# Performance work log

Hardware: AMD Instinct MI355X
Metric: run time of the kernel (lower is better)

The kernel has to match this reference:

```python
import jax, jax.numpy as jnp
import numpy as np

FACTOR = 5  # ProbAttention factor


def setup_inputs() -> dict:
    key = jax.random.key(0)
    kq, kk, kv = jax.random.split(key, 3)
    B, H, D, L = 4, 8, 64, 4096
    return {
        "queries": jax.random.normal(kq, (B, H, D, L), jnp.float32),
        "keys": jax.random.normal(kk, (B, H, D, L), jnp.float32),
        "values": jax.random.normal(kv, (B, H, D, L), jnp.float32),
        "attn_mask": jnp.zeros((1,), jnp.bool_),  # unused when mask_flag=True (recomputed internally)
    }


def reference(queries, keys, values, attn_mask):
    B, H, D, L_Q = queries.shape  # input layout [B, H, D, L]
    q = jnp.transpose(queries, (0, 1, 3, 2))  # [B,H,L,D]
    k = jnp.transpose(keys, (0, 1, 3, 2))
    v = jnp.transpose(values, (0, 1, 3, 2))
    L_K = k.shape[2]  # true key length (used inside _prob_QK)
    # --- faithful bug from original: L_K/L_V read from queries' LAST dim (=D) ---
    L_K_bug = D
    L_V_bug = D
    U_part = FACTOR * int(np.ceil(np.log(L_K_bug)))
    U_part = U_part if U_part < L_K_bug else L_K_bug  # sample_k
    u = FACTOR * int(np.ceil(np.log(L_Q)))
    u = u if u < L_Q else L_Q  # n_top
    # scaling (bugged denominators for k, v)
    q = q / (np.sqrt(D) * np.sqrt(L_Q))
    k = k / (np.sqrt(D) * np.sqrt(L_K_bug))
    v = v / (np.sqrt(D) * np.sqrt(L_V_bug))

    # ---- _prob_QK: sampled QK, top-u query selection ----
    skey = jax.random.key(42)  # fixed key: deterministic stand-in for torch.randint
    index_sample = jax.random.randint(skey, (L_Q, U_part), 0, L_K)  # [L_Q, U_part]
    K_sample = k[:, :, index_sample, :]  # [B,H,L_Q,U_part,D]
    Q_K_sample = jnp.einsum('bhld,bhlsd->bhls', q, K_sample)  # [B,H,L_Q,U_part]
    M = Q_K_sample.max(-1) - Q_K_sample.sum(-1) / L_K  # sparsity measure, real L_K here
    _, M_top = jax.lax.top_k(M, u)  # [B,H,u] (order irrelevant: distinct scatter targets)
    Q_reduce = jnp.take_along_axis(q, M_top[..., None], axis=2)  # [B,H,u,D]
    scores = jnp.einsum('bhud,bhkd->bhuk', Q_reduce, k)  # [B,H,u,L_K]

    scale = 1.0 / (np.sqrt(D) * np.sqrt(L_Q))  # self.scale is None
    scores = scores * scale

    # ---- initial context (mask_flag=True -> causal cumsum) ----
    context = jnp.cumsum(v, axis=2)  # [B,H,L_Q,D]

    # ---- ProbMask + update ----
    causal = jnp.triu(jnp.ones((L_Q, L_K), jnp.bool_), 1)  # [L_Q, L_K]
    indicator = causal[M_top]  # [B,H,u,L_K]
    scores = jnp.where(indicator, -jnp.inf, scores)
    attn = jax.nn.softmax(scores, axis=-1)
    upd = jnp.einsum('bhuk,bhkd->bhud', attn, v)  # [B,H,u,D]
    bi = jnp.arange(B)[:, None, None]
    hi = jnp.arange(H)[None, :, None]
    context = context.at[bi, hi, M_top].set(upd)

    out = jnp.transpose(context, (0, 1, 3, 2)).reshape(queries.shape)
    return out
```

## Files before the change

### kernel.cpp

```cpp
#include <hip/hip_runtime.h>
#include <cstdint>

constexpr int B_ = 4, H_ = 8, D_ = 64, L_ = 4096;
constexpr int BH = B_ * H_;
constexpr int U_PART = 25;
constexpr int TOPU = 45;
constexpr int CHUNK = 128;
constexpr int NCH = L_ / CHUNK;
constexpr int PSTRIDE = 68;

#define JAX_THREEFRY_PARTITIONABLE 1

__host__ __device__ inline void tf2x32(uint32_t k0, uint32_t k1,
                                       uint32_t x0, uint32_t x1,
                                       uint32_t& y0, uint32_t& y1) {
  const uint32_t ks2 = k0 ^ k1 ^ 0x1BD11BDAu;
  uint32_t v0 = x0 + k0, v1 = x1 + k1;
#define RND(r) { v0 += v1; v1 = (v1 << (r)) | (v1 >> (32 - (r))); v1 ^= v0; }
  RND(13) RND(15) RND(26) RND(6)
  v0 += k1; v1 += ks2 + 1u;
  RND(17) RND(29) RND(16) RND(24)
  v0 += ks2; v1 += k0 + 2u;
  RND(13) RND(15) RND(26) RND(6)
  v0 += k0; v1 += k1 + 3u;
  RND(17) RND(29) RND(16) RND(24)
  v0 += k1; v1 += ks2 + 4u;
  RND(13) RND(15) RND(26) RND(6)
  v0 += ks2; v1 += k0 + 5u;
#undef RND
  y0 = v0; y1 = v1;
}

__global__ __launch_bounds__(256) void sample_idx_kernel(int* __restrict__ idx,
                                                         uint32_t k2a, uint32_t k2b) {
#if JAX_THREEFRY_PARTITIONABLE
  int i = blockIdx.x * 256 + threadIdx.x;
  if (i >= L_ * U_PART) return;
  uint32_t y0, y1;
  tf2x32(k2a, k2b, 0u, (uint32_t)i, y0, y1);
  idx[i] = (int)((y0 ^ y1) & 4095u);
#else
  int j = blockIdx.x * 256 + threadIdx.x;
  const int half = (L_ * U_PART) / 2;
  if (j >= half) return;
  uint32_t y0, y1;
  tf2x32(k2a, k2b, (uint32_t)j, (uint32_t)(j + half), y0, y1);
  idx[j] = (int)(y0 & 4095u);
  idx[j + half] = (int)(y1 & 4095u);
#endif
}

__global__ __launch_bounds__(256) void transpose_cumsum(
    const float* __restrict__ q, const float* __restrict__ k, const float* __restrict__ v,
    float* __restrict__ qt, float* __restrict__ kt, float* __restrict__ out) {
  const int bh = blockIdx.y;
  const int t = threadIdx.x;
  if (blockIdx.z == 2) {
    const int row = bh * D_ + blockIdx.x;
    const float* src = v + (size_t)row * L_;
    float* dst = out + (size_t)row * L_;
    float vals[16];
    const float4* s4 = (const float4*)(src + t * 16);
#pragma unroll
    for (int i = 0; i < 4; i++) {
      float4 x = s4[i];
      vals[4 * i + 0] = x.x; vals[4 * i + 1] = x.y;
      vals[4 * i + 2] = x.z; vals[4 * i + 3] = x.w;
    }
    float run = 0.0f;
#pragma unroll
    for (int i = 0; i < 16; i++) { run += vals[i] * (1.0f / 64.0f); vals[i] = run; }
    float x = run;
#pragma unroll
    for (int off = 1; off < 64; off <<= 1) {
      float y = __shfl_up(x, off, 64);
      if ((t & 63) >= off) x += y;
    }
    __shared__ float wtot[4];
    if ((t & 63) == 63) wtot[t >> 6] = x;
    __syncthreads();
    float woff = 0.0f;
    for (int w = 0; w < (t >> 6); w++) woff += wtot[w];
    const float excl = x - run + woff;
#pragma unroll
    for (int i = 0; i < 16; i++) vals[i] += excl;
    float4* d4 = (float4*)(dst + t * 16);
#pragma unroll
    for (int i = 0; i < 4; i++)
      d4[i] = make_float4(vals[4 * i], vals[4 * i + 1], vals[4 * i + 2], vals[4 * i + 3]);
    return;
  }
  const float* src; float* dst; float scale;
  if (blockIdx.z == 0) { src = q; dst = qt; scale = 1.0f / 512.0f; }
  else                 { src = k; dst = kt; scale = 1.0f / 64.0f; }
  const int l0 = blockIdx.x * 64;
  __shared__ float tile[64][65];
  const float* s = src + (size_t)bh * D_ * L_ + l0;
  float* d = dst + (size_t)bh * L_ * D_;
  const int rhi = t >> 4, rlo = t & 15;
#pragma unroll
  for (int i = 0; i < 4; i++) {
    const int dd = i * 16 + rhi;
    float4 x = *(const float4*)&s[(size_t)dd * L_ + 4 * rlo];
    tile[dd][4 * rlo + 0] = x.x * scale;
    tile[dd][4 * rlo + 1] = x.y * scale;
    tile[dd][4 * rlo + 2] = x.z * scale;
    tile[dd][4 * rlo + 3] = x.w * scale;
  }
  __syncthreads();
#pragma unroll
  for (int i = 0; i < 4; i++) {
    const int ll = i * 16 + rhi;
    float4 o;
    o.x = tile[4 * rlo + 0][ll];
    o.y = tile[4 * rlo + 1][ll];
    o.z = tile[4 * rlo + 2][ll];
    o.w = tile[4 * rlo + 3][ll];
    *(float4*)&d[(size_t)(l0 + ll) * D_ + 4 * rlo] = o;
  }
}

__device__ __forceinline__ float dpp_bcast_add16(float x) {
  int xi;
  xi = __builtin_amdgcn_mov_dpp(__float_as_int(x), 0x140, 0xF, 0xF, true);
  x += __int_as_float(xi);
  xi = __builtin_amdgcn_mov_dpp(__float_as_int(x), 0x141, 0xF, 0xF, true);
  x += __int_as_float(xi);
  xi = __builtin_amdgcn_mov_dpp(__float_as_int(x), 0x4E, 0xF, 0xF, true);
  x += __int_as_float(xi);
  xi = __builtin_amdgcn_mov_dpp(__float_as_int(x), 0xB1, 0xF, 0xF, true);
  x += __int_as_float(xi);
  return x;
}

__global__ __launch_bounds__(256) void m_kernel(const float* __restrict__ qt,
                                                const float* __restrict__ kt,
                                                const int* __restrict__ idx,
                                                float* __restrict__ M) {
  const int t = threadIdx.x;
  const int w = t >> 6, lane = t & 63;
  const int g = lane >> 4, gl = lane & 15;
  const int xcd = blockIdx.x & 7;
  const int slot = blockIdx.x >> 3;
  const int bh = xcd * 4 + (slot >> 8);
  const int lg = slot & 255;
  const int l = lg * 16 + w * 4 + g;
  const int gidx = bh * L_ + l;
  const float* qtb = qt + (size_t)bh * L_ * D_;
  const float* ktb = kt + (size_t)bh * L_ * D_;
  const float4 ql = *(const float4*)(qtb + (size_t)l * D_ + gl * 4);
  const int* ip = idx + l * U_PART;
  float mx = -INFINITY, sm = 0.0f;
#pragma unroll 5
  for (int s = 0; s < U_PART; s++) {
    int ki = ip[s];
    float4 kk = *(const float4*)(ktb + (size_t)ki * D_ + gl * 4);
    float p = ql.x * kk.x + ql.y * kk.y + ql.z * kk.z + ql.w * kk.w;
    p = dpp_bcast_add16(p);
    mx = fmaxf(mx, p);
    sm += p;
  }
  if (gl == 0) M[gidx] = mx - sm * (1.0f / 4096.0f);
}

__global__ __launch_bounds__(256) void topk_kernel(const float* __restrict__ M,
                                                   int* __restrict__ ssel_g) {
  const int bh = blockIdx.x, t = threadIdx.x;
  const int w = t >> 6, lane = t & 63;
  const float* Mb = M + (size_t)bh * L_;
  const int base = w * 1024 + lane;
  uint32_t v[16];
#pragma unroll
  for (int j = 0; j < 16; j++) {
    uint32_t b = __float_as_uint(Mb[base + j * 64]);
    v[j] = b ^ ((b & 0x80000000u) ? 0xFFFFFFFFu : 0x80000000u);
  }
  __shared__ unsigned long long red[4];
  __shared__ int picks[TOPU];
  for (int it = 0; it < TOPU; it++) {
    unsigned long long best = 0ull;
#pragma unroll
    for (int j = 0; j < 16; j++) {
      unsigned long long key = ((unsigned long long)v[j] << 32)
                             | (uint32_t)(L_ - 1 - (base + j * 64));
      best = (key > best) ? key : best;
    }
#pragma unroll
    for (int off = 32; off; off >>= 1) {
      unsigned long long o = __shfl_xor(best, off, 64);
      best = (o > best) ? o : best;
    }
    if (lane == 0) red[w] = best;
    __syncthreads();
    unsigned long long g = red[0];
    if (red[1] > g) g = red[1];
    if (red[2] > g) g = red[2];
    if (red[3] > g) g = red[3];
    const int bi = L_ - 1 - (int)(g & 0xFFFFFFFFu);
    if (t == 0) picks[it] = bi;
    if ((bi >> 10) == w && (bi & 63) == lane) {
      const int slot = (bi >> 6) & 15;
#pragma unroll
      for (int j = 0; j < 16; j++) if (slot == j) v[j] = 0u;
    }
    __syncthreads();
  }
  if (t < TOPU) {
    int my = picks[t];
    int rank = 0;
    for (int j = 0; j < TOPU; j++) rank += (picks[j] > my);
    ssel_g[bh * TOPU + rank] = my;
  }
}

__global__ __launch_bounds__(256) void update_partial(const float* __restrict__ qt,
                                                      const float* __restrict__ kraw,
                                                      const float* __restrict__ vraw,
                                                      const int* __restrict__ ssel_g,
                                                      float* __restrict__ part) {
  const int xcd = blockIdx.x & 7;
  const int slot = blockIdx.x >> 3;
  const int bh = xcd * 4 + (slot >> 4);
  const int ch0 = slot & 15;
  const int t = threadIdx.x;
  const int w = t >> 6, lane = t & 63;
  const int kl = lane & 15, rg = lane >> 4;

  __shared__ float kv[CHUNK * 64];
  __shared__ float qs[48 * 68];
  __shared__ float eS[48 * 132];
  __shared__ int ssel[48];

  if (t < 48) ssel[t] = (t < TOPU) ? ssel_g[bh * TOPU + t] : -1;
  __syncthreads();

#pragma unroll
  for (int j = 0; j < 3; j++) {
    int it = t + 256 * j;
    int rr = it >> 4, dc = it & 15;
    int sel = ssel[rr];
    float4 qv = make_float4(0.f, 0.f, 0.f, 0.f);
    if (sel >= 0) qv = *(const float4*)&qt[((size_t)bh * L_ + sel) * D_ + 4 * dc];
    *(float4*)&qs[rr * 68 + 4 * dc] = qv;
  }

  for (int pass = 0; pass < 2; pass++) {
    const int ch = pass ? (31 - ch0) : ch0;
    const int k0 = ch * CHUNK;
    int lo = 0, hi = TOPU;
    while (lo < hi) { int mid = (lo + hi) >> 1; if (ssel[mid] >= k0) lo = mid + 1; else hi = mid; }
    const int nact = lo;
    if (nact == 0) continue;

    __syncthreads();
    const float* kb = kraw + (size_t)bh * D_ * L_ + k0;
#pragma unroll
    for (int j = 0; j < 8; j++) {
      int e4 = 4 * (t + 256 * j);
      int d = e4 >> 7, key = e4 & 127;
      *(float4*)&kv[e4] = *(const float4*)&kb[(size_t)d * L_ + key];
    }
    __syncthreads();

    const int wr0 = 12 * w;
    if (wr0 < nact) {
      float s[3][8];
#pragma unroll
      for (int j = 0; j < 3; j++)
#pragma unroll
        for (int x = 0; x < 8; x++) s[j][x] = 0.f;
#pragma unroll 8
      for (int d = 0; d < 64; d++) {
        float4 ka = *(const float4*)&kv[d * 128 + 4 * kl];
        float4 kb2 = *(const float4*)&kv[d * 128 + 64 + 4 * kl];
#pragma unroll
        for (int j = 0; j < 3; j++) {
          float qd = qs[(wr0 + 3 * rg + j) * 68 + d];
          s[j][0] += qd * ka.x;  s[j][1] += qd * ka.y;
          s[j][2] += qd * ka.z;  s[j][3] += qd * ka.w;
          s[j][4] += qd * kb2.x; s[j][5] += qd * kb2.y;
          s[j][6] += qd * kb2.z; s[j][7] += qd * kb2.w;
        }
      }
#pragma unroll
      for (int j = 0; j < 3; j++) {
        const int R = wr0 + 3 * rg + j;
        const int sel = ssel[R];
        float mx = -INFINITY;
#pragma unroll
        for (int x = 0; x < 8; x++) {
          int kg = k0 + 4 * kl + (x < 4 ? x : 60 + x);
          s[j][x] *= (1.0f / 32768.0f);
          if (kg > sel) s[j][x] = -INFINITY;
          mx = fmaxf(mx, s[j][x]);
        }
        mx = fmaxf(mx, __shfl_xor(mx, 1, 64));
        mx = fmaxf(mx, __shfl_xor(mx, 2, 64));
        mx = fmaxf(mx, __shfl_xor(mx, 4, 64));
        mx = fmaxf(mx, __shfl_xor(mx, 8, 64));
        float e[8], sm = 0.f;
#pragma unroll
        for (int x = 0; x < 8; x++) { e[x] = expf(s[j][x] - mx); sm += e[x]; }
        sm += __shfl_xor(sm, 1, 64);
        sm += __shfl_xor(sm, 2, 64);
        sm += __shfl_xor(sm, 4, 64);
        sm += __shfl_xor(sm, 8, 64);
        *(float4*)&eS[R * 132 + 4 * kl] = make_float4(e[0], e[1], e[2], e[3]);
        *(float4*)&eS[R * 132 + 64 + 4 * kl] = make_float4(e[4], e[5], e[6], e[7]);
        if (kl == 0 && R < nact) {
          float* p = part + ((size_t)(bh * TOPU + R) * NCH + ch) * PSTRIDE;
          p[64] = mx; p[65] = sm;
        }
      }
    }
    __syncthreads();
    const float* vb = vraw + (size_t)bh * D_ * L_ + k0;
#pragma unroll
    for (int j = 0; j < 8; j++) {
      int e4 = 4 * (t + 256 * j);
      int d = e4 >> 7, kq = (e4 & 127) >> 2;
      float4 vv = *(const float4*)&vb[(size_t)d * L_ + 4 * kq];
      *(float4*)&kv[d * 128 + ((kq ^ (d & 31)) << 2)] = vv;
    }
    __syncthreads();
    if (wr0 < nact) {
      float acc[3][4];
#pragma unroll
      for (int j = 0; j < 3; j++)
#pragma unroll
        for (int x = 0; x < 4; x++) acc[j][x] = 0.f;
      const int dbase = 4 * kl;
#pragma unroll 4
      for (int kb = 0; kb < 32; kb++) {
        float4 ev[3];
#pragma unroll
        for (int j = 0; j < 3; j++)
          ev[j] = *(const float4*)&eS[(wr0 + 3 * rg + j) * 132 + 4 * kb];
#pragma unroll
        for (int x = 0; x < 4; x++) {
          const int dx = dbase + x;
          float4 vv = *(const float4*)&kv[dx * 128 + ((kb ^ (dx & 31)) << 2)];
#pragma unroll
          for (int j = 0; j < 3; j++) {
            acc[j][x] += ev[j].x * vv.x + ev[j].y * vv.y
                       + ev[j].z * vv.z + ev[j].w * vv.w;
          }
        }
      }
#pragma unroll
      for (int j = 0; j < 3; j++) {
        const int R = wr0 + 3 * rg + j;
        if (R < nact) {
          float* p = part + ((size_t)(bh * TOPU + R) * NCH + ch) * PSTRIDE;
          float4 o = make_float4(acc[j][0] * (1.0f / 64.0f), acc[j][1] * (1.0f / 64.0f),
                                 acc[j][2] * (1.0f / 64.0f), acc[j][3] * (1.0f / 64.0f));
          *(float4*)&p[4 * kl] = o;
        }
      }
    }
  }
}

__global__ __launch_bounds__(256) void update_combine(const float* __restrict__ part,
                                                      const int* __restrict__ ssel_g,
                                                      float* __restrict__ out) {
  const int row = blockIdx.x * 4 + (threadIdx.x >> 6);
  if (row >= BH * TOPU) return;
  const int bh = row / TOPU;
  const int sel = ssel_g[row];
  const int d = threadIdx.x & 63;
  const int nv = sel / CHUNK + 1;
  const float* p = part + (size_t)row * NCH * PSTRIDE;

  float m = -INFINITY;
  for (int c = 0; c < nv; c++) m = fmaxf(m, p[c * PSTRIDE + 64]);

  float num = 0.0f, den = 0.0f;
  for (int c = 0; c < nv; c++) {
    float mc = p[c * PSTRIDE + 64];
    float wgt = expf(mc - m);
    num += wgt * p[c * PSTRIDE + d];
    den += wgt * p[c * PSTRIDE + 65];
  }
  out[((size_t)bh * D_ + d) * L_ + sel] = num / den;
}

extern "C" void kernel_launch(void* const* d_in, const int* in_sizes, int n_in,
                              void* d_out, int out_size, void* d_ws, size_t ws_size,
                              hipStream_t stream) {
  const float* q = (const float*)d_in[0];
  const float* k = (const float*)d_in[1];
  const float* v = (const float*)d_in[2];
  float* out = (float*)d_out;

  const size_t NT = (size_t)BH * L_ * D_;
  float* qt = (float*)d_ws;
  float* kt = qt + NT;
  float* M  = kt + NT;
  int* idx  = (int*)(M + (size_t)BH * L_);
  int* ssel = idx + L_ * U_PART;
  float* part = (float*)(ssel + BH * TOPU);

  uint32_t k2a, k2b;
#if JAX_THREEFRY_PARTITIONABLE
  tf2x32(0u, 42u, 0u, 1u, k2a, k2b);
#else
  uint32_t a0, a1, b0, b1;
  tf2x32(0u, 42u, 0u, 2u, a0, a1);
  tf2x32(0u, 42u, 1u, 3u, b0, b1);
  k2a = a1; k2b = b1;
#endif

#if JAX_THREEFRY_PARTITIONABLE
  sample_idx_kernel<<<(L_ * U_PART + 255) / 256, 256, 0, stream>>>(idx, k2a, k2b);
#else
  sample_idx_kernel<<<(L_ * U_PART / 2 + 255) / 256, 256, 0, stream>>>(idx, k2a, k2b);
#endif
  transpose_cumsum<<<dim3(L_ / 64, BH, 3), 256, 0, stream>>>(q, k, v, qt, kt, out);
  m_kernel<<<BH * L_ / 16, 256, 0, stream>>>(qt, kt, idx, M);
  topk_kernel<<<BH, 256, 0, stream>>>(M, ssel);
  update_partial<<<BH * 16, 256, 0, stream>>>(qt, k, v, ssel, part);
  update_combine<<<(BH * TOPU + 3) / 4, 256, 0, stream>>>(part, ssel, out);
}
```

Before: 171.1 us.

## Fuse Q transpose into M kernel and fold index sampling into cumsum blocks

Removes the global transposed copy of Q. The M kernel now transposes and scales its own 64-row Q tile in shared memory and processes four query rows per group. The top-k kernel gathers and scales the selected query rows into a small buffer for the update stage. The random sample-index generation moves into the cumsum blocks of the transpose kernel, which drops one kernel launch and a full write and read of Q. The cost is more work per block in the M kernel, and the top-k gather does strided reads from raw Q.

```diff
diff --git a/kernel.cpp b/kernel.cpp
--- a/kernel.cpp
+++ b/kernel.cpp
@@ -31,31 +31,32 @@
   y0 = v0; y1 = v1;
 }
 
-__global__ __launch_bounds__(256) void sample_idx_kernel(int* __restrict__ idx,
-                                                         uint32_t k2a, uint32_t k2b) {
-#if JAX_THREEFRY_PARTITIONABLE
-  int i = blockIdx.x * 256 + threadIdx.x;
-  if (i >= L_ * U_PART) return;
-  uint32_t y0, y1;
-  tf2x32(k2a, k2b, 0u, (uint32_t)i, y0, y1);
-  idx[i] = (int)((y0 ^ y1) & 4095u);
-#else
-  int j = blockIdx.x * 256 + threadIdx.x;
-  const int half = (L_ * U_PART) / 2;
-  if (j >= half) return;
-  uint32_t y0, y1;
-  tf2x32(k2a, k2b, (uint32_t)j, (uint32_t)(j + half), y0, y1);
-  idx[j] = (int)(y0 & 4095u);
-  idx[j + half] = (int)(y1 & 4095u);
-#endif
-}
-
 __global__ __launch_bounds__(256) void transpose_cumsum(
-    const float* __restrict__ q, const float* __restrict__ k, const float* __restrict__ v,
-    float* __restrict__ qt, float* __restrict__ kt, float* __restrict__ out) {
+    const float* __restrict__ k, const float* __restrict__ v,
+    float* __restrict__ kt, float* __restrict__ out,
+    int* __restrict__ idx, uint32_t k2a, uint32_t k2b) {
   const int bh = blockIdx.y;
   const int t = threadIdx.x;
-  if (blockIdx.z == 2) {
+  if (blockIdx.z == 1) {
+#if JAX_THREEFRY_PARTITIONABLE
+    const int bid = bh * 64 + blockIdx.x;
+    if (t < 50) {
+      uint32_t y0, y1;
+      const uint32_t i = (uint32_t)(bid * 50 + t);
+      tf2x32(k2a, k2b, 0u, i, y0, y1);
+      idx[bid * 50 + t] = (int)((y0 ^ y1) & 4095u);
+    }
+#else
+    const int bid = bh * 64 + blockIdx.x;
+    const int half = (L_ * U_PART) / 2;
+    if (t < 25) {
+      uint32_t y0, y1;
+      const int j = bid * 25 + t;
+      tf2x32(k2a, k2b, (uint32_t)j, (uint32_t)(j + half), y0, y1);
+      idx[j] = (int)(y0 & 4095u);
+      idx[j + half] = (int)(y1 & 4095u);
+    }
+#endif
     const int row = bh * D_ + blockIdx.x;
     const float* src = v + (size_t)row * L_;
     float* dst = out + (size_t)row * L_;
@@ -90,22 +91,19 @@
       d4[i] = make_float4(vals[4 * i], vals[4 * i + 1], vals[4 * i + 2], vals[4 * i + 3]);
     return;
   }
-  const float* src; float* dst; float scale;
-  if (blockIdx.z == 0) { src = q; dst = qt; scale = 1.0f / 512.0f; }
-  else                 { src = k; dst = kt; scale = 1.0f / 64.0f; }
   const int l0 = blockIdx.x * 64;
   __shared__ float tile[64][65];
-  const float* s = src + (size_t)bh * D_ * L_ + l0;
-  float* d = dst + (size_t)bh * L_ * D_;
+  const float* s = k + (size_t)bh * D_ * L_ + l0;
+  float* d = kt + (size_t)bh * L_ * D_;
   const int rhi = t >> 4, rlo = t & 15;
 #pragma unroll
   for (int i = 0; i < 4; i++) {
     const int dd = i * 16 + rhi;
     float4 x = *(const float4*)&s[(size_t)dd * L_ + 4 * rlo];
-    tile[dd][4 * rlo + 0] = x.x * scale;
-    tile[dd][4 * rlo + 1] = x.y * scale;
-    tile[dd][4 * rlo + 2] = x.z * scale;
-    tile[dd][4 * rlo + 3] = x.w * scale;
+    tile[dd][4 * rlo + 0] = x.x * (1.0f / 64.0f);
+    tile[dd][4 * rlo + 1] = x.y * (1.0f / 64.0f);
+    tile[dd][4 * rlo + 2] = x.z * (1.0f / 64.0f);
+    tile[dd][4 * rlo + 3] = x.w * (1.0f / 64.0f);
   }
   __syncthreads();
 #pragma unroll
@@ -133,7 +131,7 @@
   return x;
 }
 
-__global__ __launch_bounds__(256) void m_kernel(const float* __restrict__ qt,
+__global__ __launch_bounds__(256) void m_kernel(const float* __restrict__ qraw,
                                                 const float* __restrict__ kt,
                                                 const int* __restrict__ idx,
                                                 float* __restrict__ M) {
@@ -142,29 +140,49 @@
   const int g = lane >> 4, gl = lane & 15;
   const int xcd = blockIdx.x & 7;
   const int slot = blockIdx.x >> 3;
-  const int bh = xcd * 4 + (slot >> 8);
-  const int lg = slot & 255;
-  const int l = lg * 16 + w * 4 + g;
-  const int gidx = bh * L_ + l;
-  const float* qtb = qt + (size_t)bh * L_ * D_;
+  const int bh = xcd * 4 + (slot >> 6);
+  const int l0 = (slot & 63) * 64;
   const float* ktb = kt + (size_t)bh * L_ * D_;
-  const float4 ql = *(const float4*)(qtb + (size_t)l * D_ + gl * 4);
-  const int* ip = idx + l * U_PART;
-  float mx = -INFINITY, sm = 0.0f;
+  __shared__ float qs[64][65];
+  {
+    const float* s = qraw + (size_t)bh * D_ * L_ + l0;
+    const int rhi = t >> 4, rlo = t & 15;
+#pragma unroll
+    for (int i = 0; i < 4; i++) {
+      const int dd = i * 16 + rhi;
+      float4 x = *(const float4*)&s[(size_t)dd * L_ + 4 * rlo];
+      qs[4 * rlo + 0][dd] = x.x * (1.0f / 512.0f);
+      qs[4 * rlo + 1][dd] = x.y * (1.0f / 512.0f);
+      qs[4 * rlo + 2][dd] = x.z * (1.0f / 512.0f);
+      qs[4 * rlo + 3][dd] = x.w * (1.0f / 512.0f);
+    }
+  }
+  __syncthreads();
+#pragma unroll
+  for (int r = 0; r < 4; r++) {
+    const int ll = r * 16 + w * 4 + g;
+    const int l = l0 + ll;
+    const float q0 = qs[ll][4 * gl + 0], q1 = qs[ll][4 * gl + 1];
+    const float q2 = qs[ll][4 * gl + 2], q3 = qs[ll][4 * gl + 3];
+    const int* ip = idx + l * U_PART;
+    float mx = -INFINITY, sm = 0.0f;
 #pragma unroll 5
-  for (int s = 0; s < U_PART; s++) {
-    int ki = ip[s];
-    float4 kk = *(const float4*)(ktb + (size_t)ki * D_ + gl * 4);
-    float p = ql.x * kk.x + ql.y * kk.y + ql.z * kk.z + ql.w * kk.w;
-    p = dpp_bcast_add16(p);
-    mx = fmaxf(mx, p);
-    sm += p;
-  }
-  if (gl == 0) M[gidx] = mx - sm * (1.0f / 4096.0f);
+    for (int s2 = 0; s2 < U_PART; s2++) {
+      const int ki = ip[s2];
+      float4 kk = *(const float4*)(ktb + (size_t)ki * D_ + gl * 4);
+      float p = q0 * kk.x + q1 * kk.y + q2 * kk.z + q3 * kk.w;
+      p = dpp_bcast_add16(p);
+      mx = fmaxf(mx, p);
+      sm += p;
+    }
+    if (gl == 0) M[bh * L_ + l] = mx - sm * (1.0f / 4096.0f);
+  }
 }
 
 __global__ __launch_bounds__(256) void topk_kernel(const float* __restrict__ M,
-                                                   int* __restrict__ ssel_g) {
+                                                   const float* __restrict__ qraw,
+                                                   int* __restrict__ ssel_g,
+                                                   float* __restrict__ qsel) {
   const int bh = blockIdx.x, t = threadIdx.x;
   const int w = t >> 6, lane = t & 63;
   const float* Mb = M + (size_t)bh * L_;
@@ -177,6 +195,7 @@
   }
   __shared__ unsigned long long red[4];
   __shared__ int picks[TOPU];
+  __shared__ int ssorted[TOPU];
   for (int it = 0; it < TOPU; it++) {
     unsigned long long best = 0ull;
 #pragma unroll
@@ -209,11 +228,19 @@
     int my = picks[t];
     int rank = 0;
     for (int j = 0; j < TOPU; j++) rank += (picks[j] > my);
-    ssel_g[bh * TOPU + rank] = my;
-  }
-}
-
-__global__ __launch_bounds__(256) void update_partial(const float* __restrict__ qt,
+    ssorted[rank] = my;
+  }
+  __syncthreads();
+  if (t < TOPU) ssel_g[bh * TOPU + t] = ssorted[t];
+  const float* qb = qraw + (size_t)bh * D_ * L_;
+  for (int e = t; e < TOPU * 64; e += 256) {
+    const int r = e >> 6, d = e & 63;
+    qsel[((size_t)bh * TOPU + r) * 64 + e % 64] =
+        qb[(size_t)d * L_ + ssorted[r]] * (1.0f / 512.0f);
+  }
+}
+
+__global__ __launch_bounds__(256) void update_partial(const float* __restrict__ qsel,
                                                       const float* __restrict__ kraw,
                                                       const float* __restrict__ vraw,
                                                       const int* __restrict__ ssel_g,
@@ -238,9 +265,8 @@
   for (int j = 0; j < 3; j++) {
     int it = t + 256 * j;
     int rr = it >> 4, dc = it & 15;
-    int sel = ssel[rr];
     float4 qv = make_float4(0.f, 0.f, 0.f, 0.f);
-    if (sel >= 0) qv = *(const float4*)&qt[((size_t)bh * L_ + sel) * D_ + 4 * dc];
+    if (rr < TOPU) qv = *(const float4*)&qsel[((size_t)bh * TOPU + rr) * 64 + 4 * dc];
     *(float4*)&qs[rr * 68 + 4 * dc] = qv;
   }
 
@@ -394,12 +420,12 @@
   float* out = (float*)d_out;
 
   const size_t NT = (size_t)BH * L_ * D_;
-  float* qt = (float*)d_ws;
-  float* kt = qt + NT;
+  float* kt = (float*)d_ws;
   float* M  = kt + NT;
   int* idx  = (int*)(M + (size_t)BH * L_);
   int* ssel = idx + L_ * U_PART;
-  float* part = (float*)(ssel + BH * TOPU);
+  float* qsel = (float*)(ssel + BH * TOPU);
+  float* part = qsel + (size_t)BH * TOPU * 64;
 
   uint32_t k2a, k2b;
 #if JAX_THREEFRY_PARTITIONABLE
@@ -411,14 +437,9 @@
   k2a = a1; k2b = b1;
 #endif
 
-#if JAX_THREEFRY_PARTITIONABLE
-  sample_idx_kernel<<<(L_ * U_PART + 255) / 256, 256, 0, stream>>>(idx, k2a, k2b);
-#else
-  sample_idx_kernel<<<(L_ * U_PART / 2 + 255) / 256, 256, 0, stream>>>(idx, k2a, k2b);
-#endif
-  transpose_cumsum<<<dim3(L_ / 64, BH, 3), 256, 0, stream>>>(q, k, v, qt, kt, out);
-  m_kernel<<<BH * L_ / 16, 256, 0, stream>>>(qt, kt, idx, M);
-  topk_kernel<<<BH, 256, 0, stream>>>(M, ssel);
-  update_partial<<<BH * 16, 256, 0, stream>>>(qt, k, v, ssel, part);
+  transpose_cumsum<<<dim3(L_ / 64, BH, 2), 256, 0, stream>>>(k, v, kt, out, idx, k2a, k2b);
+  m_kernel<<<BH * 64, 256, 0, stream>>>(q, kt, idx, M);
+  topk_kernel<<<BH, 256, 0, stream>>>(M, q, ssel, qsel);
+  update_partial<<<BH * 16, 256, 0, stream>>>(qsel, k, v, ssel, part);
   update_combine<<<(BH * TOPU + 3) / 4, 256, 0, stream>>>(part, ssel, out);
 }
```

Result: faster. 165.0 us (-3.6%).
